# Kernel tuning notes

Measured on AMD Instinct MI355X. Metric: run time of the kernel, lower is better.

## Reference

```python
import jax, jax.numpy as jnp
import numpy as np

Q_N = 65536   # queries
KV_N = 65536  # keys/values
C = 256       # channels
H = 8         # heads
D = C // H
N_E = 524288  # edges
SCALE = 1.0 / np.sqrt(C).astype(np.float32)  # sim_scale/sqrt(num_ch), sim_scale=1
LN_EPS = 1e-5


def setup_inputs() -> dict:
    key = jax.random.key(0)
    ks = jax.random.split(key, 8)
    q = jax.random.normal(ks[0], (Q_N, C), jnp.float32)
    k = jax.random.normal(ks[1], (KV_N, C), jnp.float32)
    bias = jax.random.normal(ks[2], (N_E, H), jnp.float32) * 0.1
    src = jax.random.randint(ks[3], (N_E,), 0, KV_N)
    dst = jnp.sort(jax.random.randint(ks[4], (N_E,), 0, Q_N))
    wq = jax.random.normal(ks[5], (C, C), jnp.float32) * 0.02
    wk = jax.random.normal(ks[6], (C, C), jnp.float32) * 0.02
    wo = jax.random.normal(ks[7], (C, C), jnp.float32) * 0.02
    return {
        "q": q, "k": k, "bias": bias,
        "ln_w": jnp.ones((C,), jnp.float32), "ln_b": jnp.zeros((C,), jnp.float32),
        "wq": wq, "bq": jnp.zeros((C,), jnp.float32),
        "wk": wk, "bk": jnp.zeros((C,), jnp.float32),
        "wo": wo, "bo": jnp.zeros((C,), jnp.float32),
        "src": src, "dst": dst,
    }


def _layernorm(x, w, b):
    mu = jnp.mean(x, axis=-1, keepdims=True)
    var = jnp.var(x, axis=-1, keepdims=True)
    return (x - mu) * jax.lax.rsqrt(var + LN_EPS) * w + b


def reference(q, k, bias, ln_w, ln_b, wq, bq, wk, bk, wo, bo, src, dst):
    residual = q
    qn = _layernorm(q, ln_w, ln_b)           # norm_loc='pre'
    qp = qn @ wq.T + bq                       # [Q, C]
    kp = k @ wk.T + bk                        # [KV, C]; same_kv -> v = kp
    # gather per-edge, split heads: [N, H, D]
    qe = qp[dst].reshape(N_E, H, D)
    ke = kp[src].reshape(N_E, H, D)
    sim = (jnp.sum(qe * ke, axis=-1) + bias) * SCALE   # [N, H]
    # segment-max per dst (init -inf, matching index_reduce amax)
    max_sim = jax.ops.segment_max(sim, dst, num_segments=Q_N)  # [Q, H]
    e = jnp.exp(sim - max_sim[dst])
    wsum = 1e-8 + jax.ops.segment_sum(e, dst, num_segments=Q_N)  # [Q, H]
    weights = e / wsum[dst]                   # [N, H]
    out_e = (ke * weights[..., None]).reshape(N_E, C)  # weighted values (v=k)
    out = jax.ops.segment_sum(out_e, dst, num_segments=Q_N)  # [Q, C]
    out = out @ wo.T + bo + residual
    return out, weights
```

## Files before the change

kernel.cpp:

```cpp
#include <hip/hip_runtime.h>
#include <cmath>

#define QN    65536
#define KVN   65536
#define CD    256
#define NH    8
#define NE    524288
#define SCL   0.0625f
#define LNEPS 1e-5f
#define LOG2E 1.4426950408889634f

typedef __bf16 bf16x8 __attribute__((ext_vector_type(8)));
typedef float  f32x4  __attribute__((ext_vector_type(4)));

__device__ __forceinline__ float b2f(ushort u) {
    return __builtin_bit_cast(float, (unsigned)u << 16);
}
__device__ __forceinline__ ushort f2bf(float f) {
    unsigned u = __builtin_bit_cast(unsigned, f);
    return (ushort)((u + 0x7FFFu + ((u >> 16) & 1u)) >> 16);
}

#if __has_builtin(__builtin_amdgcn_exp2f)
__device__ __forceinline__ float fexp2(float x) { return __builtin_amdgcn_exp2f(x); }
#else
__device__ __forceinline__ float fexp2(float x) {
    float r; asm volatile("v_exp_f32 %0, %1" : "=v"(r) : "v"(x)); return r;
}
#endif

#define GLD16(g, l) __builtin_amdgcn_global_load_lds( \
    (const __attribute__((address_space(1))) unsigned int*)(const void*)(g), \
    (__attribute__((address_space(3))) unsigned int*)(void*)(l), 16, 0, 0)

#define LNB   (QN / 4)
#define RLB   (NE / 256)
__global__ __launch_bounds__(256) void prep_k(const float* __restrict__ q,
                                              const float* __restrict__ k,
                                              const float* __restrict__ lnw,
                                              const float* __restrict__ lnb,
                                              const float* __restrict__ wq,
                                              const float* __restrict__ wk,
                                              const float* __restrict__ wo,
                                              const int* __restrict__ dst,
                                              ushort* __restrict__ qn,
                                              ushort* __restrict__ kb,
                                              ushort* __restrict__ wb,
                                              int* __restrict__ row_lo) {
    const int blk = blockIdx.x;
    if (blk < LNB) {
        int row  = (blk << 2) + (threadIdx.x >> 6);
        int lane = threadIdx.x & 63;
        float4 v = *(const float4*)(q + (size_t)row * CD + (lane << 2));
        float s  = v.x + v.y + v.z + v.w;
        float s2 = v.x * v.x + v.y * v.y + v.z * v.z + v.w * v.w;
        #pragma unroll
        for (int m = 1; m < 64; m <<= 1) {
            s  += __shfl_xor(s, m);
            s2 += __shfl_xor(s2, m);
        }
        float mu   = s * (1.0f / CD);
        float rstd = rsqrtf(s2 * (1.0f / CD) - mu * mu + LNEPS);
        float4 w = *(const float4*)(lnw + (lane << 2));
        float4 b = *(const float4*)(lnb + (lane << 2));
        ushort4 o;
        o.x = f2bf((v.x - mu) * rstd * w.x + b.x);
        o.y = f2bf((v.y - mu) * rstd * w.y + b.y);
        o.z = f2bf((v.z - mu) * rstd * w.z + b.z);
        o.w = f2bf((v.w - mu) * rstd * w.w + b.w);
        *(ushort4*)(qn + (size_t)row * CD + (lane << 2)) = o;
    } else if (blk < LNB + 192) {
        int idx4 = ((blk - LNB) * 256 + threadIdx.x) * 4;
        int mat  = idx4 >> 16;
        int off  = idx4 & 65535;
        const float* src = (mat == 0) ? wq : (mat == 1) ? wk : wo;
        float4 v = *(const float4*)(src + off);
        ushort4 o;
        o.x = f2bf(v.x); o.y = f2bf(v.y); o.z = f2bf(v.z); o.w = f2bf(v.w);
        *(ushort4*)(wb + idx4) = o;
    } else if (blk < LNB + 192 + RLB) {
        int e = (blk - LNB - 192) * 256 + threadIdx.x;
        int d     = dst[e];
        int dprev = (e == 0) ? -1 : dst[e - 1];
        for (int qq = dprev + 1; qq <= d; ++qq) row_lo[qq] = e;
        if (e == NE - 1)
            for (int qq = d + 1; qq <= QN; ++qq) row_lo[qq] = NE;
    } else {
        int row  = ((blk - LNB - 192 - RLB) << 2) + (threadIdx.x >> 6);
        int lane = threadIdx.x & 63;
        float4 v = *(const float4*)(k + (size_t)row * CD + (lane << 2));
        ushort4 o;
        o.x = f2bf(v.x); o.y = f2bf(v.y); o.z = f2bf(v.z); o.w = f2bf(v.w);
        *(ushort4*)(kb + (size_t)row * CD + (lane << 2)) = o;
    }
}

template<int EPI, int NT>
__global__ __launch_bounds__(512) void gemm2_k(const ushort* __restrict__ A0,
                                               const ushort* __restrict__ A1,
                                               const ushort* __restrict__ B0,
                                               const ushort* __restrict__ B1,
                                               const float* __restrict__ bias0,
                                               const float* __restrict__ bias1,
                                               const float* __restrict__ resid,
                                               void* __restrict__ C0,
                                               void* __restrict__ C1) {
    const bool second = (blockIdx.z != 0);
    const ushort* Ap   = second ? A1 : A0;
    const ushort* B    = second ? B1 : B0;
    const float*  bias = second ? bias1 : bias0;
    void*         Cout = second ? C1 : C0;

    __shared__ __align__(16) ushort Bs[8][4096];
    __shared__ __align__(16) ushort As[8][4096];

    const int t    = threadIdx.x;
    const int lane = t & 63;
    const int wid  = t >> 6;
    const int wm   = wid & 1;
    const int wn   = wid >> 1;
    const size_t bn  = (size_t)blockIdx.y * 128;
    size_t bm = (size_t)blockIdx.x * (NT * 128);

    const int sr = t >> 2;
    const int sc = (t & 3) * 8;

    constexpr int E = (EPI == 0) ? 8 : 16;

    f32x4 acc[4][2] = {};
    f32x4 biasv[2];
    #pragma unroll
    for (int ni = 0; ni < 2; ++ni)
        biasv[ni] = *(const f32x4*)(bias + bn + wn * 32 + ni * 16 + ((lane >> 4) << 2));

    #pragma unroll
    for (int s = 0; s < 8; ++s)
        GLD16(B + (bn + sr) * CD + (s << 5) + sc, &Bs[s][wid << 9]);
    #pragma unroll
    for (int s = 0; s < 6; ++s)
        GLD16(Ap + (bm + sr) * CD + (s << 5) + sc, &As[s][wid << 9]);
    asm volatile("" : "+v"(biasv[0]), "+v"(biasv[1]));

#define KSTEP(KT, VM, GUARD)                                                          \
  {                                                                                   \
    if (GUARD) {                                                                      \
      const ushort* ga_ = Ap + (bm + (((KT) >= 2) ? 128 : 0) + sr) * CD               \
                          + ((((KT) + 6) & 7) << 5) + sc;                             \
      GLD16(ga_, &As[((KT) + 6) & 7][wid << 9]);                                      \
    }                                                                                 \
    asm volatile("s_waitcnt vmcnt(%0) lgkmcnt(0)\n\ts_barrier" :: "i"(VM) : "memory");\
    {                                                                                 \
      const int kq_ = (lane >> 4) << 3;                                               \
      bf16x8 af_[4], bg_[2];                                                          \
      _Pragma("unroll")                                                               \
      for (int mi = 0; mi < 4; ++mi)                                                  \
        af_[mi] = *(const bf16x8*)&As[(KT) & 7][((wm * 64 + mi * 16 + (lane & 15)) << 5) + kq_]; \
      _Pragma("unroll")                                                               \
      for (int ni = 0; ni < 2; ++ni)                                                  \
        bg_[ni] = *(const bf16x8*)&Bs[(KT)][((wn * 32 + ni * 16 + (lane & 15)) << 5) + kq_];     \
      _Pragma("unroll")                                                               \
      for (int mi = 0; mi < 4; ++mi)                                                  \
        _Pragma("unroll")                                                             \
        for (int ni = 0; ni < 2; ++ni)                                                \
          acc[mi][ni] = __builtin_amdgcn_mfma_f32_16x16x32_bf16(bg_[ni], af_[mi], acc[mi][ni], 0, 0, 0); \
    }                                                                                 \
  }

#define EPILOG()                                                                      \
  {                                                                                   \
    _Pragma("unroll")                                                                 \
    for (int mi = 0; mi < 4; ++mi) {                                                  \
      const size_t row_ = bm + wm * 64 + mi * 16 + (lane & 15);                       \
      _Pragma("unroll")                                                               \
      for (int ni = 0; ni < 2; ++ni) {                                                \
        const size_t col_ = bn + wn * 32 + ni * 16 + ((lane >> 4) << 2);              \
        if (EPI == 0) {                                                               \
          ushort4 o_;                                                                 \
          o_.x = f2bf(acc[mi][ni][0] + biasv[ni][0]);                                 \
          o_.y = f2bf(acc[mi][ni][1] + biasv[ni][1]);                                 \
          o_.z = f2bf(acc[mi][ni][2] + biasv[ni][2]);                                 \
          o_.w = f2bf(acc[mi][ni][3] + biasv[ni][3]);                                 \
          *(ushort4*)((ushort*)Cout + row_ * CD + col_) = o_;                         \
        } else {                                                                      \
          f32x4 rs_ = *(const f32x4*)(resid + row_ * CD + col_);                      \
          f32x4 o_;                                                                   \
          o_[0] = acc[mi][ni][0] + biasv[ni][0] + rs_[0];                             \
          o_[1] = acc[mi][ni][1] + biasv[ni][1] + rs_[1];                             \
          o_[2] = acc[mi][ni][2] + biasv[ni][2] + rs_[2];                             \
          o_[3] = acc[mi][ni][3] + biasv[ni][3] + rs_[3];                             \
          *(f32x4*)((float*)Cout + row_ * CD + col_) = o_;                            \
        }                                                                             \
        acc[mi][ni] = (f32x4){0.f, 0.f, 0.f, 0.f};                                    \
      }                                                                               \
    }                                                                                 \
    asm volatile("" ::: "memory");          \
  }

    KSTEP(0, 6, 1) KSTEP(1, 6, 1) KSTEP(2, 6, 1) KSTEP(3, 6, 1)
    KSTEP(4, 6, 1) KSTEP(5, 6, 1) KSTEP(6, 6, 1) KSTEP(7, 6, 1)
    EPILOG();
    bm += 128;

    for (int tt = 1; tt < NT - 1; ++tt) {
        KSTEP(0, 6 + E, 1) KSTEP(1, 6 + E, 1) KSTEP(2, 6 + E, 1) KSTEP(3, 6 + E, 1)
        KSTEP(4, 6 + E, 1) KSTEP(5, 6 + E, 1) KSTEP(6, 6, 1)     KSTEP(7, 6, 1)
        EPILOG();
        bm += 128;
    }

    KSTEP(0, 6 + E, 1) KSTEP(1, 6 + E, 1) KSTEP(2, 5 + E, 0) KSTEP(3, 4 + E, 0)
    KSTEP(4, 3 + E, 0) KSTEP(5, 2 + E, 0) KSTEP(6, 1, 0)     KSTEP(7, 0, 0)
    EPILOG();

#undef KSTEP
#undef EPILOG
}

__global__ __launch_bounds__(64) void edge_attn_k(const ushort* __restrict__ qp,
                                                  const ushort* __restrict__ kp,
                                                  const float* __restrict__ bias,
                                                  const int* __restrict__ src,
                                                  const int* __restrict__ row_lo,
                                                  ushort* __restrict__ ao,
                                                  float* __restrict__ simw) {
    const int q    = blockIdx.x;
    const int lane = threadIdx.x;
    const int lo = row_lo[q];
    const int hi = row_lo[q + 1];
    const int deg = hi - lo;
    const float SC2 = SCL * LOG2E;

    ushort4 qu = *(const ushort4*)(qp + (size_t)q * CD + (lane << 2));
    float4 qv = {b2f(qu.x) * SC2, b2f(qu.y) * SC2, b2f(qu.z) * SC2, b2f(qu.w) * SC2};
    float4 acc = {0.f, 0.f, 0.f, 0.f};
    float m = -INFINITY, s = 0.f;
    float wval0 = 0.f, wval1 = 0.f;

    for (int base = lo; base < hi; base += 8) {
        const int cnum = (base - lo) >> 3;
        int sv = 0;
        if (lane < 8 && base + lane < hi) sv = src[base + lane];
        float bch = 0.f;
        if (lane < (hi - base) * 8) bch = bias[(size_t)base * NH + lane] * SC2;
        ushort4 ku[8];
        #pragma unroll
        for (int i = 0; i < 8; ++i) {
            if (base + i < hi) {
                int sidx = __shfl(sv, i);
                ku[i] = *(const ushort4*)(kp + (size_t)sidx * CD + (lane << 2));
            }
        }
        #pragma unroll
        for (int i = 0; i < 8; ++i) {
            if (base + i < hi) {
                float4 kv = {b2f(ku[i].x), b2f(ku[i].y), b2f(ku[i].z), b2f(ku[i].w)};
                float d = qv.x * kv.x + qv.y * kv.y + qv.z * kv.z + qv.w * kv.w;
                d += __shfl_xor(d, 1);
                d += __shfl_xor(d, 2);
                d += __shfl_xor(d, 4);
                float bvi = __shfl(bch, (i << 3) + (lane >> 3));
                float sim = d + bvi;
                float tw = __shfl(sim, (lane & 7) << 3);
                bool mine = ((lane >> 3) == i);
                if (deg <= 16) {
                    if (cnum == 0) wval0 = mine ? tw : wval0;
                    else           wval1 = mine ? tw : wval1;
                } else {
                    wval0 = mine ? tw : wval0;
                }
                float mnew  = fmaxf(m, sim);
                float scale = fexp2(m - mnew);
                float ex    = fexp2(sim - mnew);
                s = s * scale + ex;
                acc.x = acc.x * scale + ex * kv.x;
                acc.y = acc.y * scale + ex * kv.y;
                acc.z = acc.z * scale + ex * kv.z;
                acc.w = acc.w * scale + ex * kv.w;
                m = mnew;
            }
        }
        if (deg > 16) {
            int lim = hi - base; if (lim > 8) lim = 8;
            if (lane < lim * 8) simw[(size_t)base * NH + lane] = wval0;
        }
    }

    float ws  = s + 1e-8f;
    float inv = 1.0f / ws;
    ushort4 o;
    o.x = f2bf(acc.x * inv);
    o.y = f2bf(acc.y * inv);
    o.z = f2bf(acc.z * inv);
    o.w = f2bf(acc.w * inv);
    *(ushort4*)(ao + (size_t)q * CD + (lane << 2)) = o;

    if (deg > 0) {
        const float mm = __shfl(m,   (lane & 7) << 3);
        const float ii = __shfl(inv, (lane & 7) << 3);
        if (deg <= 8) {
            if (lane < deg * 8)
                simw[(size_t)lo * NH + lane] = fexp2(wval0 - mm) * ii;
        } else if (deg <= 16) {
            simw[(size_t)lo * NH + lane] = fexp2(wval0 - mm) * ii;
            if (lane < (deg - 8) * 8)
                simw[(size_t)(lo + 8) * NH + lane] = fexp2(wval1 - mm) * ii;
        } else {
            asm volatile("s_waitcnt vmcnt(0)" ::: "memory");
            for (int i = lane; i < deg * 8; i += 64) {
                size_t idx = (size_t)lo * NH + i;
                float v = simw[idx];
                simw[idx] = fexp2(v - mm) * ii;
            }
        }
    }
}

extern "C" void kernel_launch(void* const* d_in, const int* in_sizes, int n_in,
                              void* d_out, int out_size, void* d_ws, size_t ws_size,
                              hipStream_t stream) {
    const float* q    = (const float*)d_in[0];
    const float* k    = (const float*)d_in[1];
    const float* bias = (const float*)d_in[2];
    const float* lnw  = (const float*)d_in[3];
    const float* lnb  = (const float*)d_in[4];
    const float* wq   = (const float*)d_in[5];
    const float* bq   = (const float*)d_in[6];
    const float* wk   = (const float*)d_in[7];
    const float* bk   = (const float*)d_in[8];
    const float* wo   = (const float*)d_in[9];
    const float* bo   = (const float*)d_in[10];
    const int*   src  = (const int*)d_in[11];
    const int*   dst  = (const int*)d_in[12];

    float* out_m = (float*)d_out;
    float* out_w = out_m + (size_t)QN * CD;

    ushort* qn_b = (ushort*)d_ws;
    ushort* qp_b = qn_b + (size_t)QN * CD;
    ushort* kp_b = qp_b + (size_t)QN * CD;
    ushort* wb   = kp_b + (size_t)KVN * CD;
    int*    rowlo = (int*)(wb + 3 * 65536);

    ushort* kb = (ushort*)d_out;

    prep_k<<<dim3(LNB + 192 + RLB + LNB), dim3(256), 0, stream>>>(
        q, k, lnw, lnb, wq, wk, wo, dst, qn_b, kb, wb, rowlo);

    gemm2_k<0, 8><<<dim3(64, 2, 2), dim3(512), 0, stream>>>(
        qn_b, kb, wb, wb + 65536, bq, bk, nullptr, qp_b, kp_b);

    edge_attn_k<<<dim3(QN), dim3(64), 0, stream>>>(
        qp_b, kp_b, bias, src, rowlo, qn_b , out_w);

    gemm2_k<1, 4><<<dim3(128, 2, 1), dim3(512), 0, stream>>>(
        qn_b, qn_b, wb + 131072, wb + 131072, bo, bo, q, out_m, out_m);
}
```

Baseline: 170.1 us.

## Fuse K fp32-to-bf16 conversion into projection GEMM A-operand loads

Removes the separate K conversion pass from the prep kernel. The K-projection GEMM blocks now load fp32 K straight into registers, convert it to bf16 and store it to LDS, with a register-prefetched software pipeline two k-steps ahead. This drops one 64K x 256 bf16 write and read-back through global memory. In exchange those blocks lose async global-to-LDS loads and take on extra VALU conversion work plus register pressure, and every k-step now waits on a barrier.

```diff
diff --git a/kernel.cpp b/kernel.cpp
--- a/kernel.cpp
+++ b/kernel.cpp
@@ -36,7 +36,6 @@
 #define LNB   (QN / 4)
 #define RLB   (NE / 256)
 __global__ __launch_bounds__(256) void prep_k(const float* __restrict__ q,
-                                              const float* __restrict__ k,
                                               const float* __restrict__ lnw,
                                               const float* __restrict__ lnb,
                                               const float* __restrict__ wq,
@@ -44,7 +43,6 @@
                                               const float* __restrict__ wo,
                                               const int* __restrict__ dst,
                                               ushort* __restrict__ qn,
-                                              ushort* __restrict__ kb,
                                               ushort* __restrict__ wb,
                                               int* __restrict__ row_lo) {
     const int blk = blockIdx.x;
@@ -78,26 +76,19 @@
         ushort4 o;
         o.x = f2bf(v.x); o.y = f2bf(v.y); o.z = f2bf(v.z); o.w = f2bf(v.w);
         *(ushort4*)(wb + idx4) = o;
-    } else if (blk < LNB + 192 + RLB) {
+    } else {
         int e = (blk - LNB - 192) * 256 + threadIdx.x;
         int d     = dst[e];
         int dprev = (e == 0) ? -1 : dst[e - 1];
         for (int qq = dprev + 1; qq <= d; ++qq) row_lo[qq] = e;
         if (e == NE - 1)
             for (int qq = d + 1; qq <= QN; ++qq) row_lo[qq] = NE;
-    } else {
-        int row  = ((blk - LNB - 192 - RLB) << 2) + (threadIdx.x >> 6);
-        int lane = threadIdx.x & 63;
-        float4 v = *(const float4*)(k + (size_t)row * CD + (lane << 2));
-        ushort4 o;
-        o.x = f2bf(v.x); o.y = f2bf(v.y); o.z = f2bf(v.z); o.w = f2bf(v.w);
-        *(ushort4*)(kb + (size_t)row * CD + (lane << 2)) = o;
     }
 }
 
 template<int EPI, int NT>
 __global__ __launch_bounds__(512) void gemm2_k(const ushort* __restrict__ A0,
-                                               const ushort* __restrict__ A1,
+                                               const float* __restrict__ Afp,
                                                const ushort* __restrict__ B0,
                                                const ushort* __restrict__ B1,
                                                const float* __restrict__ bias0,
@@ -105,11 +96,11 @@
                                                const float* __restrict__ resid,
                                                void* __restrict__ C0,
                                                void* __restrict__ C1) {
-    const bool second = (blockIdx.z != 0);
-    const ushort* Ap   = second ? A1 : A0;
-    const ushort* B    = second ? B1 : B0;
-    const float*  bias = second ? bias1 : bias0;
-    void*         Cout = second ? C1 : C0;
+    const bool conv = (blockIdx.z != 0);
+    const ushort* Ap   = A0;
+    const ushort* B    = conv ? B1 : B0;
+    const float*  bias = conv ? bias1 : bias0;
+    void*         Cout = conv ? C1 : C0;
 
     __shared__ __align__(16) ushort Bs[8][4096];
     __shared__ __align__(16) ushort As[8][4096];
@@ -133,22 +124,65 @@
     for (int ni = 0; ni < 2; ++ni)
         biasv[ni] = *(const f32x4*)(bias + bn + wn * 32 + ni * 16 + ((lane >> 4) << 2));
 
+    float4 pa0, pa1, pb0, pb1;
+
     #pragma unroll
     for (int s = 0; s < 8; ++s)
         GLD16(B + (bn + sr) * CD + (s << 5) + sc, &Bs[s][wid << 9]);
-    #pragma unroll
-    for (int s = 0; s < 6; ++s)
-        GLD16(Ap + (bm + sr) * CD + (s << 5) + sc, &As[s][wid << 9]);
+    if (conv) {
+        float4 c0[4], c1[4];
+        #pragma unroll
+        for (int s = 0; s < 4; ++s) {
+            const float* ga = Afp + (bm + sr) * CD + (s << 5) + sc;
+            c0[s] = *(const float4*)ga;
+            c1[s] = *(const float4*)(ga + 4);
+        }
+        #pragma unroll
+        for (int s = 0; s < 4; ++s) {
+            union { ushort u[8]; uint4 v; } pk;
+            pk.u[0] = f2bf(c0[s].x); pk.u[1] = f2bf(c0[s].y); pk.u[2] = f2bf(c0[s].z); pk.u[3] = f2bf(c0[s].w);
+            pk.u[4] = f2bf(c1[s].x); pk.u[5] = f2bf(c1[s].y); pk.u[6] = f2bf(c1[s].z); pk.u[7] = f2bf(c1[s].w);
+            *(uint4*)&As[s][t * 8] = pk.v;
+        }
+        { const float* ga = Afp + (bm + sr) * CD + (4 << 5) + sc; pa0 = *(const float4*)ga; pa1 = *(const float4*)(ga + 4); }
+        { const float* ga = Afp + (bm + sr) * CD + (5 << 5) + sc; pb0 = *(const float4*)ga; pb1 = *(const float4*)(ga + 4); }
+    } else {
+        #pragma unroll
+        for (int s = 0; s < 6; ++s)
+            GLD16(Ap + (bm + sr) * CD + (s << 5) + sc, &As[s][wid << 9]);
+    }
     asm volatile("" : "+v"(biasv[0]), "+v"(biasv[1]));
 
-#define KSTEP(KT, VM, GUARD)                                                          \
+#define KSTEP(KT, VM, LG, CG, FIRSTK)                                                 \
   {                                                                                   \
-    if (GUARD) {                                                                      \
-      const ushort* ga_ = Ap + (bm + (((KT) >= 2) ? 128 : 0) + sr) * CD               \
-                          + ((((KT) + 6) & 7) << 5) + sc;                             \
-      GLD16(ga_, &As[((KT) + 6) & 7][wid << 9]);                                      \
+    if (conv) {                                                                       \
+      if (CG) {                                                                       \
+        union { ushort u[8]; uint4 v; } pk_;                                          \
+        if ((KT) & 1) {                                                               \
+          pk_.u[0] = f2bf(pb0.x); pk_.u[1] = f2bf(pb0.y); pk_.u[2] = f2bf(pb0.z); pk_.u[3] = f2bf(pb0.w); \
+          pk_.u[4] = f2bf(pb1.x); pk_.u[5] = f2bf(pb1.y); pk_.u[6] = f2bf(pb1.z); pk_.u[7] = f2bf(pb1.w); \
+        } else {                                                                      \
+          pk_.u[0] = f2bf(pa0.x); pk_.u[1] = f2bf(pa0.y); pk_.u[2] = f2bf(pa0.z); pk_.u[3] = f2bf(pa0.w); \
+          pk_.u[4] = f2bf(pa1.x); pk_.u[5] = f2bf(pa1.y); pk_.u[6] = f2bf(pa1.z); pk_.u[7] = f2bf(pa1.w); \
+        }                                                                             \
+        *(uint4*)&As[((KT) + 4) & 7][t * 8] = pk_.v;                                  \
+      }                                                                               \
+      if (LG) {                                                                       \
+        const float* ga_ = Afp + (bm + (((KT) >= 2) ? 128 : 0) + sr) * CD             \
+                           + ((((KT) + 6) & 7) << 5) + sc;                            \
+        if ((KT) & 1) { pb0 = *(const float4*)ga_; pb1 = *(const float4*)(ga_ + 4); } \
+        else          { pa0 = *(const float4*)ga_; pa1 = *(const float4*)(ga_ + 4); } \
+      }                                                                               \
+      if (FIRSTK) asm volatile("s_waitcnt vmcnt(0) lgkmcnt(0)\n\ts_barrier" ::: "memory"); \
+      else        asm volatile("s_waitcnt lgkmcnt(0)\n\ts_barrier" ::: "memory");     \
+    } else {                                                                          \
+      if (LG) {                                                                       \
+        const ushort* ga_ = Ap + (bm + (((KT) >= 2) ? 128 : 0) + sr) * CD             \
+                            + ((((KT) + 6) & 7) << 5) + sc;                           \
+        GLD16(ga_, &As[((KT) + 6) & 7][wid << 9]);                                    \
+      }                                                                               \
+      asm volatile("s_waitcnt vmcnt(%0) lgkmcnt(0)\n\ts_barrier" :: "i"(VM) : "memory"); \
     }                                                                                 \
-    asm volatile("s_waitcnt vmcnt(%0) lgkmcnt(0)\n\ts_barrier" :: "i"(VM) : "memory");\
     {                                                                                 \
       const int kq_ = (lane >> 4) << 3;                                               \
       bf16x8 af_[4], bg_[2];                                                          \
@@ -193,23 +227,23 @@
         acc[mi][ni] = (f32x4){0.f, 0.f, 0.f, 0.f};                                    \
       }                                                                               \
     }                                                                                 \
-    asm volatile("" ::: "memory");          \
+    asm volatile("" ::: "memory");                                                    \
   }
 
-    KSTEP(0, 6, 1) KSTEP(1, 6, 1) KSTEP(2, 6, 1) KSTEP(3, 6, 1)
-    KSTEP(4, 6, 1) KSTEP(5, 6, 1) KSTEP(6, 6, 1) KSTEP(7, 6, 1)
+    KSTEP(0, 6, 1, 1, 1) KSTEP(1, 6, 1, 1, 0) KSTEP(2, 6, 1, 1, 0) KSTEP(3, 6, 1, 1, 0)
+    KSTEP(4, 6, 1, 1, 0) KSTEP(5, 6, 1, 1, 0) KSTEP(6, 6, 1, 1, 0) KSTEP(7, 6, 1, 1, 0)
     EPILOG();
     bm += 128;
 
     for (int tt = 1; tt < NT - 1; ++tt) {
-        KSTEP(0, 6 + E, 1) KSTEP(1, 6 + E, 1) KSTEP(2, 6 + E, 1) KSTEP(3, 6 + E, 1)
-        KSTEP(4, 6 + E, 1) KSTEP(5, 6 + E, 1) KSTEP(6, 6, 1)     KSTEP(7, 6, 1)
+        KSTEP(0, 6 + E, 1, 1, 0) KSTEP(1, 6 + E, 1, 1, 0) KSTEP(2, 6 + E, 1, 1, 0) KSTEP(3, 6 + E, 1, 1, 0)
+        KSTEP(4, 6 + E, 1, 1, 0) KSTEP(5, 6 + E, 1, 1, 0) KSTEP(6, 6, 1, 1, 0)     KSTEP(7, 6, 1, 1, 0)
         EPILOG();
         bm += 128;
     }
 
-    KSTEP(0, 6 + E, 1) KSTEP(1, 6 + E, 1) KSTEP(2, 5 + E, 0) KSTEP(3, 4 + E, 0)
-    KSTEP(4, 3 + E, 0) KSTEP(5, 2 + E, 0) KSTEP(6, 1, 0)     KSTEP(7, 0, 0)
+    KSTEP(0, 6 + E, 1, 1, 0) KSTEP(1, 6 + E, 1, 1, 0) KSTEP(2, 5 + E, 0, 1, 0) KSTEP(3, 4 + E, 0, 1, 0)
+    KSTEP(4, 3 + E, 0, 0, 0) KSTEP(5, 2 + E, 0, 0, 0) KSTEP(6, 1, 0, 0, 0)     KSTEP(7, 0, 0, 0, 0)
     EPILOG();
 
 #undef KSTEP
@@ -341,17 +375,15 @@
     ushort* wb   = kp_b + (size_t)KVN * CD;
     int*    rowlo = (int*)(wb + 3 * 65536);
 
-    ushort* kb = (ushort*)d_out;
-
-    prep_k<<<dim3(LNB + 192 + RLB + LNB), dim3(256), 0, stream>>>(
-        q, k, lnw, lnb, wq, wk, wo, dst, qn_b, kb, wb, rowlo);
+    prep_k<<<dim3(LNB + 192 + RLB), dim3(256), 0, stream>>>(
+        q, lnw, lnb, wq, wk, wo, dst, qn_b, wb, rowlo);
 
     gemm2_k<0, 8><<<dim3(64, 2, 2), dim3(512), 0, stream>>>(
-        qn_b, kb, wb, wb + 65536, bq, bk, nullptr, qp_b, kp_b);
+        qn_b, k, wb, wb + 65536, bq, bk, nullptr, qp_b, kp_b);
 
     edge_attn_k<<<dim3(QN), dim3(64), 0, stream>>>(
         qp_b, kp_b, bias, src, rowlo, qn_b , out_w);
 
     gemm2_k<1, 4><<<dim3(128, 2, 1), dim3(512), 0, stream>>>(
-        qn_b, qn_b, wb + 131072, wb + 131072, bo, bo, q, out_m, out_m);
-}
+        qn_b, nullptr, wb + 131072, wb + 131072, bo, bo, q, out_m, out_m);
+}
```

After: 186.0 us. +9.3%, slower.

## Remap edge attention lanes to (edge, head) pairs with LDS reduction

Applied to the files above, without the earlier changes.

Reworks the per-query edge attention kernel so each lane handles one (edge, head) pair and owns a full 32-channel head slice. Each lane computes its dot product locally, with no cross-lane shuffle reduction, and keeps a per-lane online softmax. The per-lane partial accumulators are then combined across the 8 edges through shared memory. This is meant to remove the serial per-edge shuffle chain and use wider 64-byte gathers per lane. In exchange it uses 32 accumulator registers per lane, a 9 KB LDS buffer and a block barrier, and does extra work on idle lanes when degree is not a multiple of 8.

```diff
diff --git a/kernel.cpp b/kernel.cpp
--- a/kernel.cpp
+++ b/kernel.cpp
@@ -15,6 +15,12 @@
 
 __device__ __forceinline__ float b2f(ushort u) {
     return __builtin_bit_cast(float, (unsigned)u << 16);
+}
+__device__ __forceinline__ float blo(unsigned u) {
+    return __builtin_bit_cast(float, u << 16);
+}
+__device__ __forceinline__ float bhi(unsigned u) {
+    return __builtin_bit_cast(float, u & 0xFFFF0000u);
 }
 __device__ __forceinline__ ushort f2bf(float f) {
     unsigned u = __builtin_bit_cast(unsigned, f);
@@ -193,7 +199,7 @@
         acc[mi][ni] = (f32x4){0.f, 0.f, 0.f, 0.f};                                    \
       }                                                                               \
     }                                                                                 \
-    asm volatile("" ::: "memory");          \
+    asm volatile("" ::: "memory");                                                    \
   }
 
     KSTEP(0, 6, 1) KSTEP(1, 6, 1) KSTEP(2, 6, 1) KSTEP(3, 6, 1)
@@ -225,91 +231,120 @@
                                                   float* __restrict__ simw) {
     const int q    = blockIdx.x;
     const int lane = threadIdx.x;
+    const int e    = lane >> 3;
+    const int h    = lane & 7;
     const int lo = row_lo[q];
     const int hi = row_lo[q + 1];
     const int deg = hi - lo;
     const float SC2 = SCL * LOG2E;
 
-    ushort4 qu = *(const ushort4*)(qp + (size_t)q * CD + (lane << 2));
-    float4 qv = {b2f(qu.x) * SC2, b2f(qu.y) * SC2, b2f(qu.z) * SC2, b2f(qu.w) * SC2};
-    float4 acc = {0.f, 0.f, 0.f, 0.f};
+    __shared__ __align__(16) float red[64 * 36];
+
+    uint4 qr[4];
+    {
+        const uint4* qrp = (const uint4*)(qp + (size_t)q * CD + (h << 5));
+        qr[0] = qrp[0]; qr[1] = qrp[1]; qr[2] = qrp[2]; qr[3] = qrp[3];
+    }
+
+    f32x4 acc4[8] = {};
     float m = -INFINITY, s = 0.f;
-    float wval0 = 0.f, wval1 = 0.f;
+    float wval0 = -INFINITY, wval1 = -INFINITY;
 
     for (int base = lo; base < hi; base += 8) {
-        const int cnum = (base - lo) >> 3;
-        int sv = 0;
-        if (lane < 8 && base + lane < hi) sv = src[base + lane];
-        float bch = 0.f;
-        if (lane < (hi - base) * 8) bch = bias[(size_t)base * NH + lane] * SC2;
-        ushort4 ku[8];
+        const bool act = (base + e) < hi;
+        int   sv = 0;
+        float bv = 0.f;
+        if (act) {
+            sv = src[base + e];
+            bv = bias[(size_t)base * NH + lane] * SC2;
+        }
+        uint4 ku[4] = {};
+        if (act) {
+            const uint4* kr = (const uint4*)(kp + (size_t)sv * CD + (h << 5));
+            ku[0] = kr[0]; ku[1] = kr[1]; ku[2] = kr[2]; ku[3] = kr[3];
+        }
+        float d = 0.f;
         #pragma unroll
-        for (int i = 0; i < 8; ++i) {
-            if (base + i < hi) {
-                int sidx = __shfl(sv, i);
-                ku[i] = *(const ushort4*)(kp + (size_t)sidx * CD + (lane << 2));
+        for (int j = 0; j < 4; ++j) {
+            const unsigned qu[4] = {qr[j].x, qr[j].y, qr[j].z, qr[j].w};
+            const unsigned kw[4] = {ku[j].x, ku[j].y, ku[j].z, ku[j].w};
+            #pragma unroll
+            for (int w = 0; w < 4; ++w) {
+                d = fmaf(blo(qu[w]), blo(kw[w]), d);
+                d = fmaf(bhi(qu[w]), bhi(kw[w]), d);
             }
         }
+        float sim = act ? fmaf(d, SC2, bv) : -INFINITY;
+
+        float cmax = sim;
+        cmax = fmaxf(cmax, __shfl_xor(cmax, 8));
+        cmax = fmaxf(cmax, __shfl_xor(cmax, 16));
+        cmax = fmaxf(cmax, __shfl_xor(cmax, 32));
+        const float mnew  = fmaxf(m, cmax);
+        const float scale = fexp2(m - mnew);
+        const float ex    = fexp2(sim - mnew);
+        s = s * scale + ex;
         #pragma unroll
-        for (int i = 0; i < 8; ++i) {
-            if (base + i < hi) {
-                float4 kv = {b2f(ku[i].x), b2f(ku[i].y), b2f(ku[i].z), b2f(ku[i].w)};
-                float d = qv.x * kv.x + qv.y * kv.y + qv.z * kv.z + qv.w * kv.w;
-                d += __shfl_xor(d, 1);
-                d += __shfl_xor(d, 2);
-                d += __shfl_xor(d, 4);
-                float bvi = __shfl(bch, (i << 3) + (lane >> 3));
-                float sim = d + bvi;
-                float tw = __shfl(sim, (lane & 7) << 3);
-                bool mine = ((lane >> 3) == i);
-                if (deg <= 16) {
-                    if (cnum == 0) wval0 = mine ? tw : wval0;
-                    else           wval1 = mine ? tw : wval1;
-                } else {
-                    wval0 = mine ? tw : wval0;
-                }
-                float mnew  = fmaxf(m, sim);
-                float scale = fexp2(m - mnew);
-                float ex    = fexp2(sim - mnew);
-                s = s * scale + ex;
-                acc.x = acc.x * scale + ex * kv.x;
-                acc.y = acc.y * scale + ex * kv.y;
-                acc.z = acc.z * scale + ex * kv.z;
-                acc.w = acc.w * scale + ex * kv.w;
-                m = mnew;
+        for (int jj = 0; jj < 8; ++jj) {
+            acc4[jj][0] *= scale; acc4[jj][1] *= scale;
+            acc4[jj][2] *= scale; acc4[jj][3] *= scale;
+        }
+        #pragma unroll
+        for (int j = 0; j < 4; ++j) {
+            const unsigned kw[4] = {ku[j].x, ku[j].y, ku[j].z, ku[j].w};
+            #pragma unroll
+            for (int w = 0; w < 4; ++w) {
+                const int qd = j * 2 + (w >> 1);
+                const int el = (w & 1) * 2;
+                acc4[qd][el]     = fmaf(ex, blo(kw[w]), acc4[qd][el]);
+                acc4[qd][el + 1] = fmaf(ex, bhi(kw[w]), acc4[qd][el + 1]);
             }
         }
-        if (deg > 16) {
-            int lim = hi - base; if (lim > 8) lim = 8;
-            if (lane < lim * 8) simw[(size_t)base * NH + lane] = wval0;
-        }
-    }
-
-    float ws  = s + 1e-8f;
-    float inv = 1.0f / ws;
+        m = mnew;
+
+        if (deg <= 16) {
+            if (base == lo) wval0 = sim; else wval1 = sim;
+        } else if (act) {
+            simw[(size_t)base * NH + lane] = sim;
+        }
+    }
+
+    s += __shfl_xor(s, 8);
+    s += __shfl_xor(s, 16);
+    s += __shfl_xor(s, 32);
+    const float inv = 1.0f / (s + 1e-8f);
+
+    #pragma unroll
+    for (int jj = 0; jj < 8; ++jj)
+        *(f32x4*)&red[lane * 36 + jj * 4] = acc4[jj];
+    __syncthreads();
+    f32x4 sum = {};
+    #pragma unroll
+    for (int ep = 0; ep < 8; ++ep) {
+        const f32x4 p = *(const f32x4*)&red[((ep << 3) + h) * 36 + (e << 2)];
+        sum[0] += p[0]; sum[1] += p[1]; sum[2] += p[2]; sum[3] += p[3];
+    }
     ushort4 o;
-    o.x = f2bf(acc.x * inv);
-    o.y = f2bf(acc.y * inv);
-    o.z = f2bf(acc.z * inv);
-    o.w = f2bf(acc.w * inv);
-    *(ushort4*)(ao + (size_t)q * CD + (lane << 2)) = o;
+    o.x = f2bf(sum[0] * inv);
+    o.y = f2bf(sum[1] * inv);
+    o.z = f2bf(sum[2] * inv);
+    o.w = f2bf(sum[3] * inv);
+    *(ushort4*)(ao + (size_t)q * CD + (h << 5) + (e << 2)) = o;
 
     if (deg > 0) {
-        const float mm = __shfl(m,   (lane & 7) << 3);
-        const float ii = __shfl(inv, (lane & 7) << 3);
         if (deg <= 8) {
-            if (lane < deg * 8)
-                simw[(size_t)lo * NH + lane] = fexp2(wval0 - mm) * ii;
+            if (lane < (deg << 3))
+                simw[(size_t)lo * NH + lane] = fexp2(wval0 - m) * inv;
         } else if (deg <= 16) {
-            simw[(size_t)lo * NH + lane] = fexp2(wval0 - mm) * ii;
-            if (lane < (deg - 8) * 8)
-                simw[(size_t)(lo + 8) * NH + lane] = fexp2(wval1 - mm) * ii;
+            simw[(size_t)lo * NH + lane] = fexp2(wval0 - m) * inv;
+            if (lane < ((deg - 8) << 3))
+                simw[(size_t)(lo + 8) * NH + lane] = fexp2(wval1 - m) * inv;
         } else {
             asm volatile("s_waitcnt vmcnt(0)" ::: "memory");
             for (int i = lane; i < deg * 8; i += 64) {
                 size_t idx = (size_t)lo * NH + i;
                 float v = simw[idx];
-                simw[idx] = fexp2(v - mm) * ii;
+                simw[idx] = fexp2(v - m) * inv;
             }
         }
     }
```

New measurement: 175.9 us. 1.03x slower.

## Process two queries per wavefront with chunked online softmax in edge attention

Applied to the files above, without the earlier changes.

The edge attention kernel now handles two query rows per 64-lane block, interleaving their gathered key loads to raise memory-level parallelism. The lane mapping changes so each lane owns a head and a slice of its channels. The dot-product reduction is batched across the 8 edges of a chunk, and the online softmax rescales once per chunk instead of once per edge. This cuts shuffle and exp counts but adds register pressure and possible imbalance when the two rows have different degrees.

```diff
diff --git a/kernel.cpp b/kernel.cpp
--- a/kernel.cpp
+++ b/kernel.cpp
@@ -15,6 +15,12 @@
 
 __device__ __forceinline__ float b2f(ushort u) {
     return __builtin_bit_cast(float, (unsigned)u << 16);
+}
+__device__ __forceinline__ float blo(unsigned u) {
+    return __builtin_bit_cast(float, u << 16);
+}
+__device__ __forceinline__ float bhi(unsigned u) {
+    return __builtin_bit_cast(float, u & 0xFFFF0000u);
 }
 __device__ __forceinline__ ushort f2bf(float f) {
     unsigned u = __builtin_bit_cast(unsigned, f);
@@ -193,7 +199,7 @@
         acc[mi][ni] = (f32x4){0.f, 0.f, 0.f, 0.f};                                    \
       }                                                                               \
     }                                                                                 \
-    asm volatile("" ::: "memory");          \
+    asm volatile("" ::: "memory");                                                    \
   }
 
     KSTEP(0, 6, 1) KSTEP(1, 6, 1) KSTEP(2, 6, 1) KSTEP(3, 6, 1)
@@ -223,93 +229,155 @@
                                                   const int* __restrict__ row_lo,
                                                   ushort* __restrict__ ao,
                                                   float* __restrict__ simw) {
-    const int q    = blockIdx.x;
     const int lane = threadIdx.x;
-    const int lo = row_lo[q];
-    const int hi = row_lo[q + 1];
-    const int deg = hi - lo;
+    const int e    = lane >> 3;
+    const int h    = lane & 7;
+    const int q0   = blockIdx.x << 1;
+    const int q1   = q0 + 1;
+    const int lo0  = row_lo[q0];
+    const int mid  = row_lo[q0 + 1];
+    const int hi1  = row_lo[q0 + 2];
+    const int hi0  = mid, lo1 = mid;
+    const int deg0 = hi0 - lo0, deg1 = hi1 - lo1;
     const float SC2 = SCL * LOG2E;
 
-    ushort4 qu = *(const ushort4*)(qp + (size_t)q * CD + (lane << 2));
-    float4 qv = {b2f(qu.x) * SC2, b2f(qu.y) * SC2, b2f(qu.z) * SC2, b2f(qu.w) * SC2};
-    float4 acc = {0.f, 0.f, 0.f, 0.f};
-    float m = -INFINITY, s = 0.f;
-    float wval0 = 0.f, wval1 = 0.f;
-
-    for (int base = lo; base < hi; base += 8) {
-        const int cnum = (base - lo) >> 3;
-        int sv = 0;
-        if (lane < 8 && base + lane < hi) sv = src[base + lane];
-        float bch = 0.f;
-        if (lane < (hi - base) * 8) bch = bias[(size_t)base * NH + lane] * SC2;
-        ushort4 ku[8];
-        #pragma unroll
-        for (int i = 0; i < 8; ++i) {
-            if (base + i < hi) {
-                int sidx = __shfl(sv, i);
-                ku[i] = *(const ushort4*)(kp + (size_t)sidx * CD + (lane << 2));
+    const uint2 qvA = *(const uint2*)(qp + (size_t)q0 * CD + (h << 5) + (e << 2));
+    const uint2 qvB = *(const uint2*)(qp + (size_t)q1 * CD + (h << 5) + (e << 2));
+
+    f32x4 accA = {0.f, 0.f, 0.f, 0.f}, accB = {0.f, 0.f, 0.f, 0.f};
+    float mA = -INFINITY, sA = 0.f, mB = -INFINITY, sB = 0.f;
+    float wA0 = -INFINITY, wA1 = -INFINITY, wB0 = -INFINITY, wB1 = -INFINITY;
+
+#define QLOAD(ON, BASE, HI, SV, BV, KU)                                               \
+    int   SV = 0;                                                                     \
+    float BV = 0.f;                                                                   \
+    uint2 KU[8];                                                                      \
+    _Pragma("unroll")                                                                 \
+    for (int ep = 0; ep < 8; ++ep) { KU[ep].x = 0u; KU[ep].y = 0u; }                  \
+    if (ON) {                                                                         \
+        if (lane < 8 && (BASE) + lane < (HI)) SV = src[(BASE) + lane];                \
+        if (lane < ((HI) - (BASE)) * 8) BV = bias[(size_t)(BASE) * NH + lane] * SC2;  \
+        _Pragma("unroll")                                                             \
+        for (int ep = 0; ep < 8; ++ep) {                                              \
+            if ((BASE) + ep < (HI)) {                                                 \
+                int sidx_ = __shfl(SV, ep);                                           \
+                KU[ep] = *(const uint2*)(kp + (size_t)sidx_ * CD + (h << 5) + (e << 2)); \
+            }                                                                         \
+        }                                                                             \
+    }
+
+#define QCHUNK(QV, KU, BV, BASE, HI, LO, ACC, M, S, W0, W1, DEG)                      \
+  {                                                                                   \
+    float p_[8];                                                                      \
+    _Pragma("unroll")                                                                 \
+    for (int ep = 0; ep < 8; ++ep) {                                                  \
+        float d_;                                                                     \
+        d_ = blo(QV.x) * blo(KU[ep].x);                                               \
+        d_ = fmaf(bhi(QV.x), bhi(KU[ep].x), d_);                                      \
+        d_ = fmaf(blo(QV.y), blo(KU[ep].y), d_);                                      \
+        d_ = fmaf(bhi(QV.y), bhi(KU[ep].y), d_);                                      \
+        p_[ep] = d_;                                                                  \
+    }                                                                                 \
+    _Pragma("unroll")                                                                 \
+    for (int r = 8; r <= 32; r <<= 1) {                                               \
+        _Pragma("unroll")                                                             \
+        for (int ep = 0; ep < 8; ++ep)                                                \
+            p_[ep] += __shfl_xor(p_[ep], r);                                          \
+    }                                                                                 \
+    float sims_[8];                                                                   \
+    _Pragma("unroll")                                                                 \
+    for (int ep = 0; ep < 8; ++ep) {                                                  \
+        float bvp_ = __shfl(BV, (ep << 3) + h);                                       \
+        sims_[ep] = ((BASE) + ep < (HI)) ? fmaf(p_[ep], SC2, bvp_) : -INFINITY;       \
+    }                                                                                 \
+    float cmax_ = sims_[0];                                                           \
+    _Pragma("unroll")                                                                 \
+    for (int ep = 1; ep < 8; ++ep) cmax_ = fmaxf(cmax_, sims_[ep]);                   \
+    const float mnew_  = fmaxf(M, cmax_);                                             \
+    const float scale_ = fexp2(M - mnew_);                                            \
+    ACC[0] *= scale_; ACC[1] *= scale_; ACC[2] *= scale_; ACC[3] *= scale_;           \
+    float esum_ = 0.f;                                                                \
+    _Pragma("unroll")                                                                 \
+    for (int ep = 0; ep < 8; ++ep) {                                                  \
+        const float ex_ = fexp2(sims_[ep] - mnew_);                                   \
+        esum_ += ex_;                                                                 \
+        ACC[0] = fmaf(ex_, blo(KU[ep].x), ACC[0]);                                    \
+        ACC[1] = fmaf(ex_, bhi(KU[ep].x), ACC[1]);                                    \
+        ACC[2] = fmaf(ex_, blo(KU[ep].y), ACC[2]);                                    \
+        ACC[3] = fmaf(ex_, bhi(KU[ep].y), ACC[3]);                                    \
+    }                                                                                 \
+    S = S * scale_ + esum_;                                                           \
+    M = mnew_;                                                                        \
+    float ta_ = (e & 1) ? sims_[1] : sims_[0];                                        \
+    float tb_ = (e & 1) ? sims_[3] : sims_[2];                                        \
+    float tc_ = (e & 1) ? sims_[5] : sims_[4];                                        \
+    float td_ = (e & 1) ? sims_[7] : sims_[6];                                        \
+    float te_ = (e & 2) ? tb_ : ta_;                                                  \
+    float tf_ = (e & 2) ? td_ : tc_;                                                  \
+    float own_ = (e & 4) ? tf_ : te_;                                                 \
+    if ((DEG) <= 16) {                                                                \
+        if ((BASE) == (LO)) W0 = own_; else W1 = own_;                                \
+    } else if ((BASE) + e < (HI)) {                                                   \
+        simw[(size_t)(BASE) * NH + lane] = own_;                                      \
+    }                                                                                 \
+  }
+
+    int baseA = lo0, baseB = lo1;
+    const int nItA = (deg0 + 7) >> 3, nItB = (deg1 + 7) >> 3;
+    const int nIt  = nItA > nItB ? nItA : nItB;
+    for (int it = 0; it < nIt; ++it, baseA += 8, baseB += 8) {
+        const bool onA = baseA < hi0;
+        const bool onB = baseB < hi1;
+        QLOAD(onA, baseA, hi0, svA, bvA, kuA)
+        QLOAD(onB, baseB, hi1, svB, bvB, kuB)
+        if (onA) QCHUNK(qvA, kuA, bvA, baseA, hi0, lo0, accA, mA, sA, wA0, wA1, deg0)
+        if (onB) QCHUNK(qvB, kuB, bvB, baseB, hi1, lo1, accB, mB, sB, wB0, wB1, deg1)
+    }
+#undef QLOAD
+#undef QCHUNK
+
+    const float invA = 1.0f / (sA + 1e-8f);
+    const float invB = 1.0f / (sB + 1e-8f);
+
+    ushort4 oA, oB;
+    oA.x = f2bf(accA[0] * invA); oA.y = f2bf(accA[1] * invA);
+    oA.z = f2bf(accA[2] * invA); oA.w = f2bf(accA[3] * invA);
+    *(ushort4*)(ao + (size_t)q0 * CD + (h << 5) + (e << 2)) = oA;
+    oB.x = f2bf(accB[0] * invB); oB.y = f2bf(accB[1] * invB);
+    oB.z = f2bf(accB[2] * invB); oB.w = f2bf(accB[3] * invB);
+    *(ushort4*)(ao + (size_t)q1 * CD + (h << 5) + (e << 2)) = oB;
+
+    if (deg0 > 0) {
+        if (deg0 <= 8) {
+            if (lane < (deg0 << 3))
+                simw[(size_t)lo0 * NH + lane] = fexp2(wA0 - mA) * invA;
+        } else if (deg0 <= 16) {
+            simw[(size_t)lo0 * NH + lane] = fexp2(wA0 - mA) * invA;
+            if (lane < ((deg0 - 8) << 3))
+                simw[(size_t)(lo0 + 8) * NH + lane] = fexp2(wA1 - mA) * invA;
+        } else {
+            asm volatile("s_waitcnt vmcnt(0)" ::: "memory");
+            for (int i = lane; i < deg0 * 8; i += 64) {
+                size_t idx = (size_t)lo0 * NH + i;
+                float v = simw[idx];
+                simw[idx] = fexp2(v - mA) * invA;
             }
         }
-        #pragma unroll
-        for (int i = 0; i < 8; ++i) {
-            if (base + i < hi) {
-                float4 kv = {b2f(ku[i].x), b2f(ku[i].y), b2f(ku[i].z), b2f(ku[i].w)};
-                float d = qv.x * kv.x + qv.y * kv.y + qv.z * kv.z + qv.w * kv.w;
-                d += __shfl_xor(d, 1);
-                d += __shfl_xor(d, 2);
-                d += __shfl_xor(d, 4);
-                float bvi = __shfl(bch, (i << 3) + (lane >> 3));
-                float sim = d + bvi;
-                float tw = __shfl(sim, (lane & 7) << 3);
-                bool mine = ((lane >> 3) == i);
-                if (deg <= 16) {
-                    if (cnum == 0) wval0 = mine ? tw : wval0;
-                    else           wval1 = mine ? tw : wval1;
-                } else {
-                    wval0 = mine ? tw : wval0;
-                }
-                float mnew  = fmaxf(m, sim);
-                float scale = fexp2(m - mnew);
-                float ex    = fexp2(sim - mnew);
-                s = s * scale + ex;
-                acc.x = acc.x * scale + ex * kv.x;
-                acc.y = acc.y * scale + ex * kv.y;
-                acc.z = acc.z * scale + ex * kv.z;
-                acc.w = acc.w * scale + ex * kv.w;
-                m = mnew;
-            }
-        }
-        if (deg > 16) {
-            int lim = hi - base; if (lim > 8) lim = 8;
-            if (lane < lim * 8) simw[(size_t)base * NH + lane] = wval0;
-        }
-    }
-
-    float ws  = s + 1e-8f;
-    float inv = 1.0f / ws;
-    ushort4 o;
-    o.x = f2bf(acc.x * inv);
-    o.y = f2bf(acc.y * inv);
-    o.z = f2bf(acc.z * inv);
-    o.w = f2bf(acc.w * inv);
-    *(ushort4*)(ao + (size_t)q * CD + (lane << 2)) = o;
-
-    if (deg > 0) {
-        const float mm = __shfl(m,   (lane & 7) << 3);
-        const float ii = __shfl(inv, (lane & 7) << 3);
-        if (deg <= 8) {
-            if (lane < deg * 8)
-                simw[(size_t)lo * NH + lane] = fexp2(wval0 - mm) * ii;
-        } else if (deg <= 16) {
-            simw[(size_t)lo * NH + lane] = fexp2(wval0 - mm) * ii;
-            if (lane < (deg - 8) * 8)
-                simw[(size_t)(lo + 8) * NH + lane] = fexp2(wval1 - mm) * ii;
+    }
+    if (deg1 > 0) {
+        if (deg1 <= 8) {
+            if (lane < (deg1 << 3))
+                simw[(size_t)lo1 * NH + lane] = fexp2(wB0 - mB) * invB;
+        } else if (deg1 <= 16) {
+            simw[(size_t)lo1 * NH + lane] = fexp2(wB0 - mB) * invB;
+            if (lane < ((deg1 - 8) << 3))
+                simw[(size_t)(lo1 + 8) * NH + lane] = fexp2(wB1 - mB) * invB;
         } else {
             asm volatile("s_waitcnt vmcnt(0)" ::: "memory");
-            for (int i = lane; i < deg * 8; i += 64) {
-                size_t idx = (size_t)lo * NH + i;
+            for (int i = lane; i < deg1 * 8; i += 64) {
+                size_t idx = (size_t)lo1 * NH + i;
                 float v = simw[idx];
-                simw[idx] = fexp2(v - mm) * ii;
+                simw[idx] = fexp2(v - mB) * invB;
             }
         }
     }
@@ -349,7 +417,7 @@
     gemm2_k<0, 8><<<dim3(64, 2, 2), dim3(512), 0, stream>>>(
         qn_b, kb, wb, wb + 65536, bq, bk, nullptr, qp_b, kp_b);
 
-    edge_attn_k<<<dim3(QN), dim3(64), 0, stream>>>(
+    edge_attn_k<<<dim3(QN / 2), dim3(64), 0, stream>>>(
         qp_b, kp_b, bias, src, rowlo, qn_b , out_w);
 
     gemm2_k<1, 4><<<dim3(128, 2, 1), dim3(512), 0, stream>>>(
```

Result: slower. 182.1 us (+7.1%).
